# Kernel tuning notes

Hardware: AMD Instinct MI355X
Metric: run time of the kernel (lower is better)

The kernel has to match this reference:

```python
import jax, jax.numpy as jnp
import numpy as np

B, N, IN_F, H, DEG, L = 4096, 64, 32, 128, 8, 2
E = N * DEG
ALPHA = 0.2  # LeakyReLU slope
EPS = 1e-5   # LayerNorm eps


def setup_inputs() -> dict:
    key = jax.random.key(0)
    ks = jax.random.split(key, 16)
    # ring graph: node i -> (i+k) mod N for k=1..DEG (unique edges, every node has out-edges)
    src = jnp.repeat(jnp.arange(N, dtype=jnp.int32), DEG)
    dst = ((src + jnp.tile(jnp.arange(1, DEG + 1, dtype=jnp.int32), N)) % N).astype(jnp.int32)
    edge_index = jnp.stack([src, dst])  # (2, E)
    Hh = H // 2
    inp = {
        "x": jax.random.normal(ks[0], (B, IN_F), jnp.float32),
        "station_idx": jax.random.randint(ks[1], (B,), 0, N, jnp.int32),
        "edge_index": edge_index,
        "edge_weight": jax.random.uniform(ks[2], (E,), jnp.float32, 0.1, 1.0),
        "Wp": jax.random.normal(ks[3], (IN_F, H), jnp.float32) / np.sqrt(IN_F),
        "bp": jnp.zeros((H,), jnp.float32),
        "emb": jax.random.normal(ks[4], (N, Hh), jnp.float32) * 0.02,
        "gat_W": jax.random.normal(ks[5], (L, H, H), jnp.float32) / np.sqrt(H),
        "gat_a": jax.random.normal(ks[6], (L, 2 * H), jnp.float32) * 0.1,
        "W1": jax.random.normal(ks[7], (H + Hh, H), jnp.float32) / np.sqrt(H + Hh),
        "b1": jnp.zeros((H,), jnp.float32),
        "g1": jnp.ones((H,), jnp.float32),
        "be1": jnp.zeros((H,), jnp.float32),
        "W2": jax.random.normal(ks[8], (H, Hh), jnp.float32) / np.sqrt(H),
        "b2": jnp.zeros((Hh,), jnp.float32),
        "g2": jnp.ones((Hh,), jnp.float32),
        "be2": jnp.zeros((Hh,), jnp.float32),
        "Wo": jax.random.normal(ks[9], (Hh, 1), jnp.float32) / np.sqrt(Hh),
        "bo": jnp.zeros((1,), jnp.float32),
    }
    return inp


def _layernorm(v, g, b):
    m = v.mean(-1, keepdims=True)
    var = ((v - m) ** 2).mean(-1, keepdims=True)
    return (v - m) / jnp.sqrt(var + EPS) * g + b


def _gat(h, W, a, src, dst, edge_weight):
    # h: (B, N, H); W: (H, H); a: (2H,)
    Wh = jnp.einsum('bnf,fg->bng', h, W)
    s_src = Wh @ a[:H]   # (B, N)
    s_dst = Wh @ a[H:]   # (B, N)
    e = jax.nn.leaky_relu(s_src[:, src] + s_dst[:, dst], ALPHA)  # (B, E)
    e = e * edge_weight[None, :]
    att = jnp.zeros((h.shape[0], N, N), h.dtype).at[:, src, dst].set(e)
    mask = att == 0  # faithfully reproduces the torch zero-mask trick
    att = jnp.where(mask, -jnp.inf, att)
    att = jax.nn.softmax(att, axis=2)
    att = jnp.where(mask, 0.0, att)
    # dropout is identity at inference
    return jax.nn.elu(jnp.einsum('bnm,bmf->bnf', att, Wh))


def reference(x, station_idx, edge_index, edge_weight, Wp, bp, emb, gat_W, gat_a,
              W1, b1, g1, be1, W2, b2, g2, be2, Wo, bo):
    src, dst = edge_index[0], edge_index[1]
    h0 = x @ Wp + bp                               # (B, H)
    h = jnp.broadcast_to(h0[:, None, :], (x.shape[0], N, H))
    for i in range(L):
        h = h + _gat(h, gat_W[i], gat_a[i], src, dst, edge_weight)
    h_node = h[jnp.arange(x.shape[0]), station_idx]  # (B, H)
    s = emb[station_idx]                              # (B, H//2)
    z = jnp.concatenate([h_node, s], axis=-1)
    z = jax.nn.relu(_layernorm(z @ W1 + b1, g1, be1))
    z = jax.nn.relu(_layernorm(z @ W2 + b2, g2, be2))
    return (z @ Wo + bo).squeeze(-1)                  # (B,)
```

## Files before the change

### kernel.cpp

```cpp
#include <hip/hip_runtime.h>
#include <math.h>

namespace {

constexpr int INF = 32;
constexpr int H   = 128;
constexpr int HH  = 64;
constexpr int ZD  = 192;
constexpr int SPB = 4;
constexpr float LNEPS = 1e-5f;

__device__ __forceinline__ float elu1(float v) {
    return v > 0.f ? v : (__expf(v) - 1.f);
}

template<int DKq, int LDW, int NCOL>
__device__ __forceinline__ void gemm2(const float* __restrict__ W0,
                                      const float* __restrict__ act,
                                      float (&t)[SPB][NCOL])
{
    if constexpr (DKq == 8) {
        float w[8 * NCOL];
#pragma unroll
        for (int r = 0; r < 8; ++r)
#pragma unroll
            for (int c = 0; c < NCOL; ++c) w[r * NCOL + c] = W0[r * LDW + c * 64];
#pragma unroll
        for (int rr = 0; rr < 8; rr += 4) {
#pragma unroll
            for (int s = 0; s < SPB; ++s) {
                const float4 hv = *reinterpret_cast<const float4*>(act + s * ZD + rr);
#pragma unroll
                for (int c = 0; c < NCOL; ++c) {
                    t[s][c] += hv.x * w[(rr + 0) * NCOL + c] + hv.y * w[(rr + 1) * NCOL + c]
                             + hv.z * w[(rr + 2) * NCOL + c] + hv.w * w[(rr + 3) * NCOL + c];
                }
            }
        }
    } else {
        constexpr int NCH = DKq / 8;
        static_assert((NCH & 1) == 0, "even chunk count");
        float wa[8 * NCOL], wb[8 * NCOL];
#pragma unroll
        for (int r = 0; r < 8; ++r)
#pragma unroll
            for (int c = 0; c < NCOL; ++c) wa[r * NCOL + c] = W0[r * LDW + c * 64];
#pragma unroll
        for (int ch = 0; ch < NCH; ch += 2) {
#pragma unroll
            for (int r = 0; r < 8; ++r)
#pragma unroll
                for (int c = 0; c < NCOL; ++c)
                    wb[r * NCOL + c] = W0[((ch + 1) * 8 + r) * LDW + c * 64];
#pragma unroll
            for (int rr = 0; rr < 8; rr += 4) {
#pragma unroll
                for (int s = 0; s < SPB; ++s) {
                    const float4 hv = *reinterpret_cast<const float4*>(act + s * ZD + ch * 8 + rr);
#pragma unroll
                    for (int c = 0; c < NCOL; ++c) {
                        t[s][c] += hv.x * wa[(rr + 0) * NCOL + c] + hv.y * wa[(rr + 1) * NCOL + c]
                                 + hv.z * wa[(rr + 2) * NCOL + c] + hv.w * wa[(rr + 3) * NCOL + c];
                    }
                }
            }
            if (ch + 2 < NCH) {
#pragma unroll
                for (int r = 0; r < 8; ++r)
#pragma unroll
                    for (int c = 0; c < NCOL; ++c)
                        wa[r * NCOL + c] = W0[((ch + 2) * 8 + r) * LDW + c * 64];
            }
#pragma unroll
            for (int rr = 0; rr < 8; rr += 4) {
#pragma unroll
                for (int s = 0; s < SPB; ++s) {
                    const float4 hv = *reinterpret_cast<const float4*>(act + s * ZD + (ch + 1) * 8 + rr);
#pragma unroll
                    for (int c = 0; c < NCOL; ++c) {
                        t[s][c] += hv.x * wb[(rr + 0) * NCOL + c] + hv.y * wb[(rr + 1) * NCOL + c]
                                 + hv.z * wb[(rr + 2) * NCOL + c] + hv.w * wb[(rr + 3) * NCOL + c];
                    }
                }
            }
        }
    }
}

__global__ __launch_bounds__(256, 4) void fused_sthgat(
    const float* __restrict__ x, const int* __restrict__ sid,
    const float* __restrict__ Wp, const float* __restrict__ bp,
    const float* __restrict__ emb, const float* __restrict__ gatW,
    const float* __restrict__ W1, const float* __restrict__ b1,
    const float* __restrict__ g1, const float* __restrict__ be1,
    const float* __restrict__ W2, const float* __restrict__ b2,
    const float* __restrict__ g2, const float* __restrict__ be2,
    const float* __restrict__ Wo, const float* __restrict__ bo,
    float* __restrict__ out)
{
    __shared__ __align__(16) float P2[4 * SPB * H];
    __shared__ __align__(16) float buf0[SPB * ZD];
    __shared__ __align__(16) float buf1[SPB * ZD];

    const int tid  = threadIdx.x;
    const int lane = tid & 63;
    const int kq   = tid >> 6;
    const int c    = tid & 63;
    const int sw   = tid >> 6;
    const int sbase = blockIdx.x * SPB;

    if (tid < SPB * INF) {
        buf0[(tid >> 5) * ZD + (tid & 31)] = x[(size_t)sbase * INF + tid];
    }
    __syncthreads();

    {
        float t[SPB][2] = {};
        gemm2<8, H, 2>(Wp + (kq * 8) * H + c, buf0 + kq * 8, t);
#pragma unroll
        for (int s = 0; s < SPB; ++s) {
            P2[kq * (SPB * H) + s * H + c]      = t[s][0];
            P2[kq * (SPB * H) + s * H + c + 64] = t[s][1];
        }
        __syncthreads();
        float v0 = bp[c], v1 = bp[c + 64];
#pragma unroll
        for (int k = 0; k < 4; ++k) {
            v0 += P2[k * (SPB * H) + sw * H + c];
            v1 += P2[k * (SPB * H) + sw * H + c + 64];
        }
        buf1[sw * ZD + c]      = v0;
        buf1[sw * ZD + c + 64] = v1;
        __syncthreads();
    }

    {
        float t[SPB][2] = {};
        gemm2<32, H, 2>(gatW + (kq * 32) * H + c, buf1 + kq * 32, t);
#pragma unroll
        for (int s = 0; s < SPB; ++s) {
            P2[kq * (SPB * H) + s * H + c]      = t[s][0];
            P2[kq * (SPB * H) + s * H + c + 64] = t[s][1];
        }
        __syncthreads();
        float v0 = 0.f, v1 = 0.f;
#pragma unroll
        for (int k = 0; k < 4; ++k) {
            v0 += P2[k * (SPB * H) + sw * H + c];
            v1 += P2[k * (SPB * H) + sw * H + c + 64];
        }
        buf0[sw * ZD + c]      = buf1[sw * ZD + c]      + elu1(v0);
        buf0[sw * ZD + c + 64] = buf1[sw * ZD + c + 64] + elu1(v1);
        __syncthreads();
    }

    {
        float t[SPB][2] = {};
        gemm2<32, H, 2>(gatW + H * H + (kq * 32) * H + c, buf0 + kq * 32, t);
#pragma unroll
        for (int s = 0; s < SPB; ++s) {
            P2[kq * (SPB * H) + s * H + c]      = t[s][0];
            P2[kq * (SPB * H) + s * H + c + 64] = t[s][1];
        }
        __syncthreads();
        float v0 = 0.f, v1 = 0.f;
#pragma unroll
        for (int k = 0; k < 4; ++k) {
            v0 += P2[k * (SPB * H) + sw * H + c];
            v1 += P2[k * (SPB * H) + sw * H + c + 64];
        }
        buf1[sw * ZD + c]      = buf0[sw * ZD + c]      + elu1(v0);
        buf1[sw * ZD + c + 64] = buf0[sw * ZD + c + 64] + elu1(v1);
        {
            const int st = sid[sbase + sw];
            buf1[sw * ZD + H + c] = emb[st * HH + c];
        }
        __syncthreads();
    }

    {
        float t[SPB][2] = {};
        gemm2<48, H, 2>(W1 + (kq * 48) * H + c, buf1 + kq * 48, t);
#pragma unroll
        for (int s = 0; s < SPB; ++s) {
            P2[kq * (SPB * H) + s * H + c]      = t[s][0];
            P2[kq * (SPB * H) + s * H + c + 64] = t[s][1];
        }
        __syncthreads();
        float u0 = b1[c], u1 = b1[c + 64];
#pragma unroll
        for (int k = 0; k < 4; ++k) {
            u0 += P2[k * (SPB * H) + sw * H + c];
            u1 += P2[k * (SPB * H) + sw * H + c + 64];
        }
        float su = u0 + u1;
        float sq = u0 * u0 + u1 * u1;
#pragma unroll
        for (int off = 32; off >= 1; off >>= 1) {
            su += __shfl_xor(su, off, 64);
            sq += __shfl_xor(sq, off, 64);
        }
        const float m   = su * (1.f / H);
        const float var = sq * (1.f / H) - m * m;
        const float rs  = rsqrtf(var + LNEPS);
        buf0[sw * ZD + c]      = fmaxf((u0 - m) * rs * g1[c]      + be1[c],      0.f);
        buf0[sw * ZD + c + 64] = fmaxf((u1 - m) * rs * g1[c + 64] + be1[c + 64], 0.f);
        __syncthreads();
    }

    {
        float t[SPB][1] = {};
        gemm2<32, HH, 1>(W2 + (kq * 32) * HH + c, buf0 + kq * 32, t);
#pragma unroll
        for (int s = 0; s < SPB; ++s) {
            P2[kq * (SPB * HH) + s * HH + c] = t[s][0];
        }
        __syncthreads();
        float v = b2[c];
#pragma unroll
        for (int k = 0; k < 4; ++k) v += P2[k * (SPB * HH) + sw * HH + c];
        float su = v, sq = v * v;
#pragma unroll
        for (int off = 32; off >= 1; off >>= 1) {
            su += __shfl_xor(su, off, 64);
            sq += __shfl_xor(sq, off, 64);
        }
        const float m   = su * (1.f / HH);
        const float var = sq * (1.f / HH) - m * m;
        const float rs  = rsqrtf(var + LNEPS);
        const float z2  = fmaxf((v - m) * rs * g2[c] + be2[c], 0.f);
        float po = z2 * Wo[c];
#pragma unroll
        for (int off = 32; off >= 1; off >>= 1) po += __shfl_xor(po, off, 64);
        if (lane == 0) out[sbase + sw] = po + bo[0];
    }
}

}

extern "C" void kernel_launch(void* const* d_in, const int* in_sizes, int n_in,
                              void* d_out, int out_size, void* d_ws, size_t ws_size,
                              hipStream_t stream)
{
    const float* x    = (const float*)d_in[0];
    const int*   sid  = (const int*)d_in[1];
    const float* Wp   = (const float*)d_in[4];
    const float* bp   = (const float*)d_in[5];
    const float* emb  = (const float*)d_in[6];
    const float* gatW = (const float*)d_in[7];
    const float* W1   = (const float*)d_in[9];
    const float* b1   = (const float*)d_in[10];
    const float* g1   = (const float*)d_in[11];
    const float* be1  = (const float*)d_in[12];
    const float* W2   = (const float*)d_in[13];
    const float* b2   = (const float*)d_in[14];
    const float* g2   = (const float*)d_in[15];
    const float* be2  = (const float*)d_in[16];
    const float* Wo   = (const float*)d_in[17];
    const float* bo   = (const float*)d_in[18];
    float* out = (float*)d_out;

    dim3 grid(4096 / SPB);
    dim3 block(256);
    hipLaunchKernelGGL(fused_sthgat, grid, block, 0, stream,
                       x, sid, Wp, bp, emb, gatW, W1, b1, g1, be1,
                       W2, b2, g2, be2, Wo, bo, out);
}
```

Before: 104.8 us.

## Vectorize weight loads as float2 and triple-buffer weight prefetch in fused GEMMs

Result: slower. 108.4 us (+3.4%).

```diff
diff --git a/kernel.cpp b/kernel.cpp
--- a/kernel.cpp
+++ b/kernel.cpp
@@ -10,81 +10,114 @@
 constexpr int SPB = 4;
 constexpr float LNEPS = 1e-5f;
 
+template<int V> struct ic { static constexpr int value = V; };
+
+template<int N, int I = 0, class F>
+__device__ __forceinline__ void sfor(F&& f) {
+    if constexpr (I < N) { f(ic<I>{}); sfor<N, I + 1>(f); }
+}
+
 __device__ __forceinline__ float elu1(float v) {
     return v > 0.f ? v : (__expf(v) - 1.f);
 }
 
-template<int DKq, int LDW, int NCOL>
-__device__ __forceinline__ void gemm2(const float* __restrict__ W0,
-                                      const float* __restrict__ act,
-                                      float (&t)[SPB][NCOL])
+template<int DKq, int LDW>
+__device__ __forceinline__ void gemm_f2(const float* __restrict__ W0,
+                                        const float* __restrict__ actb,
+                                        float2 (&t)[SPB])
 {
-    if constexpr (DKq == 8) {
-        float w[8 * NCOL];
-#pragma unroll
-        for (int r = 0; r < 8; ++r)
-#pragma unroll
-            for (int c = 0; c < NCOL; ++c) w[r * NCOL + c] = W0[r * LDW + c * 64];
-#pragma unroll
-        for (int rr = 0; rr < 8; rr += 4) {
-#pragma unroll
-            for (int s = 0; s < SPB; ++s) {
-                const float4 hv = *reinterpret_cast<const float4*>(act + s * ZD + rr);
-#pragma unroll
-                for (int c = 0; c < NCOL; ++c) {
-                    t[s][c] += hv.x * w[(rr + 0) * NCOL + c] + hv.y * w[(rr + 1) * NCOL + c]
-                             + hv.z * w[(rr + 2) * NCOL + c] + hv.w * w[(rr + 3) * NCOL + c];
-                }
-            }
-        }
-    } else {
-        constexpr int NCH = DKq / 8;
-        static_assert((NCH & 1) == 0, "even chunk count");
-        float wa[8 * NCOL], wb[8 * NCOL];
-#pragma unroll
-        for (int r = 0; r < 8; ++r)
-#pragma unroll
-            for (int c = 0; c < NCOL; ++c) wa[r * NCOL + c] = W0[r * LDW + c * 64];
-#pragma unroll
-        for (int ch = 0; ch < NCH; ch += 2) {
-#pragma unroll
-            for (int r = 0; r < 8; ++r)
-#pragma unroll
-                for (int c = 0; c < NCOL; ++c)
-                    wb[r * NCOL + c] = W0[((ch + 1) * 8 + r) * LDW + c * 64];
-#pragma unroll
-            for (int rr = 0; rr < 8; rr += 4) {
-#pragma unroll
-                for (int s = 0; s < SPB; ++s) {
-                    const float4 hv = *reinterpret_cast<const float4*>(act + s * ZD + ch * 8 + rr);
-#pragma unroll
-                    for (int c = 0; c < NCOL; ++c) {
-                        t[s][c] += hv.x * wa[(rr + 0) * NCOL + c] + hv.y * wa[(rr + 1) * NCOL + c]
-                                 + hv.z * wa[(rr + 2) * NCOL + c] + hv.w * wa[(rr + 3) * NCOL + c];
-                    }
-                }
-            }
-            if (ch + 2 < NCH) {
-#pragma unroll
-                for (int r = 0; r < 8; ++r)
-#pragma unroll
-                    for (int c = 0; c < NCOL; ++c)
-                        wa[r * NCOL + c] = W0[((ch + 2) * 8 + r) * LDW + c * 64];
-            }
-#pragma unroll
-            for (int rr = 0; rr < 8; rr += 4) {
-#pragma unroll
-                for (int s = 0; s < SPB; ++s) {
-                    const float4 hv = *reinterpret_cast<const float4*>(act + s * ZD + (ch + 1) * 8 + rr);
-#pragma unroll
-                    for (int c = 0; c < NCOL; ++c) {
-                        t[s][c] += hv.x * wb[(rr + 0) * NCOL + c] + hv.y * wb[(rr + 1) * NCOL + c]
-                                 + hv.z * wb[(rr + 2) * NCOL + c] + hv.w * wb[(rr + 3) * NCOL + c];
-                    }
-                }
-            }
-        }
-    }
+    constexpr int NCH = DKq / 8;
+    float2 wA[8], wB[8], wC[8];
+
+    auto ld = [&](auto CH, float2 (&buf)[8]) {
+        constexpr int ch = decltype(CH)::value;
+        sfor<8>([&](auto R) {
+            buf[R.value] = *reinterpret_cast<const float2*>(
+                W0 + (size_t)(ch * 8 + R.value) * LDW);
+        });
+    };
+    auto comp = [&](auto CH, float2 (&buf)[8]) {
+        constexpr int ch = decltype(CH)::value;
+        sfor<2>([&](auto G) {
+            constexpr int g4 = decltype(G)::value;
+            constexpr int r0 = ch * 8 + g4 * 4;
+            float4 a[SPB];
+            sfor<SPB>([&](auto S) {
+                a[S.value] = *reinterpret_cast<const float4*>(
+                    actb + S.value * ZD + r0);
+            });
+            sfor<SPB>([&](auto S) {
+                constexpr int s = decltype(S)::value;
+                constexpr int rb = g4 * 4;
+                t[s].x += a[s].x * buf[rb + 0].x + a[s].y * buf[rb + 1].x
+                        + a[s].z * buf[rb + 2].x + a[s].w * buf[rb + 3].x;
+                t[s].y += a[s].x * buf[rb + 0].y + a[s].y * buf[rb + 1].y
+                        + a[s].z * buf[rb + 2].y + a[s].w * buf[rb + 3].y;
+            });
+        });
+    };
+
+    ld(ic<0>{}, wA);
+    if constexpr (NCH > 1) ld(ic<1>{}, wB);
+    sfor<NCH>([&](auto CH) {
+        constexpr int ch = decltype(CH)::value;
+        if constexpr (ch + 2 < NCH) {
+            if constexpr ((ch + 2) % 3 == 0)      ld(ic<ch + 2>{}, wA);
+            else if constexpr ((ch + 2) % 3 == 1) ld(ic<ch + 2>{}, wB);
+            else                                  ld(ic<ch + 2>{}, wC);
+        }
+        if constexpr (ch % 3 == 0)      comp(CH, wA);
+        else if constexpr (ch % 3 == 1) comp(CH, wB);
+        else                            comp(CH, wC);
+    });
+}
+
+template<int DKq, int LDW>
+__device__ __forceinline__ void gemm_s(const float* __restrict__ W0,
+                                       const float* __restrict__ actb,
+                                       float (&t)[SPB])
+{
+    constexpr int NCH = DKq / 8;
+    float wA[8], wB[8], wC[8];
+
+    auto ld = [&](auto CH, float (&buf)[8]) {
+        constexpr int ch = decltype(CH)::value;
+        sfor<8>([&](auto R) {
+            buf[R.value] = W0[(size_t)(ch * 8 + R.value) * LDW];
+        });
+    };
+    auto comp = [&](auto CH, float (&buf)[8]) {
+        constexpr int ch = decltype(CH)::value;
+        sfor<2>([&](auto G) {
+            constexpr int g4 = decltype(G)::value;
+            constexpr int r0 = ch * 8 + g4 * 4;
+            float4 a[SPB];
+            sfor<SPB>([&](auto S) {
+                a[S.value] = *reinterpret_cast<const float4*>(
+                    actb + S.value * ZD + r0);
+            });
+            sfor<SPB>([&](auto S) {
+                constexpr int s = decltype(S)::value;
+                constexpr int rb = g4 * 4;
+                t[s] += a[s].x * buf[rb + 0] + a[s].y * buf[rb + 1]
+                      + a[s].z * buf[rb + 2] + a[s].w * buf[rb + 3];
+            });
+        });
+    };
+
+    ld(ic<0>{}, wA);
+    if constexpr (NCH > 1) ld(ic<1>{}, wB);
+    sfor<NCH>([&](auto CH) {
+        constexpr int ch = decltype(CH)::value;
+        if constexpr (ch + 2 < NCH) {
+            if constexpr ((ch + 2) % 3 == 0)      ld(ic<ch + 2>{}, wA);
+            else if constexpr ((ch + 2) % 3 == 1) ld(ic<ch + 2>{}, wB);
+            else                                  ld(ic<ch + 2>{}, wC);
+        }
+        if constexpr (ch % 3 == 0)      comp(CH, wA);
+        else if constexpr (ch % 3 == 1) comp(CH, wB);
+        else                            comp(CH, wC);
+    });
 }
 
 __global__ __launch_bounds__(256, 4) void fused_sthgat(
@@ -109,90 +142,114 @@
     const int sw   = tid >> 6;
     const int sbase = blockIdx.x * SPB;
 
+    float2 wp[8];
+    sfor<8>([&](auto R) {
+        wp[R.value] = *reinterpret_cast<const float2*>(
+            Wp + (size_t)(kq * 8 + R.value) * H + 2 * c);
+    });
+    const float2 bpv = *reinterpret_cast<const float2*>(bp + 2 * c);
+
     if (tid < SPB * INF) {
         buf0[(tid >> 5) * ZD + (tid & 31)] = x[(size_t)sbase * INF + tid];
     }
     __syncthreads();
 
     {
-        float t[SPB][2] = {};
-        gemm2<8, H, 2>(Wp + (kq * 8) * H + c, buf0 + kq * 8, t);
-#pragma unroll
-        for (int s = 0; s < SPB; ++s) {
-            P2[kq * (SPB * H) + s * H + c]      = t[s][0];
-            P2[kq * (SPB * H) + s * H + c + 64] = t[s][1];
-        }
-        __syncthreads();
-        float v0 = bp[c], v1 = bp[c + 64];
-#pragma unroll
-        for (int k = 0; k < 4; ++k) {
-            v0 += P2[k * (SPB * H) + sw * H + c];
-            v1 += P2[k * (SPB * H) + sw * H + c + 64];
-        }
-        buf1[sw * ZD + c]      = v0;
-        buf1[sw * ZD + c + 64] = v1;
-        __syncthreads();
-    }
-
-    {
-        float t[SPB][2] = {};
-        gemm2<32, H, 2>(gatW + (kq * 32) * H + c, buf1 + kq * 32, t);
-#pragma unroll
-        for (int s = 0; s < SPB; ++s) {
-            P2[kq * (SPB * H) + s * H + c]      = t[s][0];
-            P2[kq * (SPB * H) + s * H + c + 64] = t[s][1];
-        }
-        __syncthreads();
-        float v0 = 0.f, v1 = 0.f;
-#pragma unroll
-        for (int k = 0; k < 4; ++k) {
-            v0 += P2[k * (SPB * H) + sw * H + c];
-            v1 += P2[k * (SPB * H) + sw * H + c + 64];
-        }
-        buf0[sw * ZD + c]      = buf1[sw * ZD + c]      + elu1(v0);
-        buf0[sw * ZD + c + 64] = buf1[sw * ZD + c + 64] + elu1(v1);
-        __syncthreads();
-    }
-
-    {
-        float t[SPB][2] = {};
-        gemm2<32, H, 2>(gatW + H * H + (kq * 32) * H + c, buf0 + kq * 32, t);
-#pragma unroll
-        for (int s = 0; s < SPB; ++s) {
-            P2[kq * (SPB * H) + s * H + c]      = t[s][0];
-            P2[kq * (SPB * H) + s * H + c + 64] = t[s][1];
-        }
-        __syncthreads();
-        float v0 = 0.f, v1 = 0.f;
-#pragma unroll
-        for (int k = 0; k < 4; ++k) {
-            v0 += P2[k * (SPB * H) + sw * H + c];
-            v1 += P2[k * (SPB * H) + sw * H + c + 64];
-        }
-        buf1[sw * ZD + c]      = buf0[sw * ZD + c]      + elu1(v0);
-        buf1[sw * ZD + c + 64] = buf0[sw * ZD + c + 64] + elu1(v1);
+        float2 t[SPB] = {};
+        const float* actb = buf0 + kq * 8;
+        sfor<2>([&](auto G) {
+            constexpr int g4 = decltype(G)::value;
+            float4 a[SPB];
+            sfor<SPB>([&](auto S) {
+                a[S.value] = *reinterpret_cast<const float4*>(
+                    actb + S.value * ZD + g4 * 4);
+            });
+            sfor<SPB>([&](auto S) {
+                constexpr int s = decltype(S)::value;
+                constexpr int rb = g4 * 4;
+                t[s].x += a[s].x * wp[rb + 0].x + a[s].y * wp[rb + 1].x
+                        + a[s].z * wp[rb + 2].x + a[s].w * wp[rb + 3].x;
+                t[s].y += a[s].x * wp[rb + 0].y + a[s].y * wp[rb + 1].y
+                        + a[s].z * wp[rb + 2].y + a[s].w * wp[rb + 3].y;
+            });
+        });
+        sfor<SPB>([&](auto S) {
+            *reinterpret_cast<float2*>(
+                P2 + kq * (SPB * H) + S.value * H + 2 * c) = t[S.value];
+        });
+        __syncthreads();
+        float2 v = bpv;
+        sfor<4>([&](auto K) {
+            const float2 p = *reinterpret_cast<const float2*>(
+                P2 + decltype(K)::value * (SPB * H) + sw * H + 2 * c);
+            v.x += p.x; v.y += p.y;
+        });
+        *reinterpret_cast<float2*>(buf1 + sw * ZD + 2 * c) = v;
+        __syncthreads();
+    }
+
+    {
+        float2 t[SPB] = {};
+        gemm_f2<32, H>(gatW + (size_t)(kq * 32) * H + 2 * c, buf1 + kq * 32, t);
+        sfor<SPB>([&](auto S) {
+            *reinterpret_cast<float2*>(
+                P2 + kq * (SPB * H) + S.value * H + 2 * c) = t[S.value];
+        });
+        __syncthreads();
+        float2 v = {0.f, 0.f};
+        sfor<4>([&](auto K) {
+            const float2 p = *reinterpret_cast<const float2*>(
+                P2 + decltype(K)::value * (SPB * H) + sw * H + 2 * c);
+            v.x += p.x; v.y += p.y;
+        });
+        const float2 hp = *reinterpret_cast<const float2*>(buf1 + sw * ZD + 2 * c);
+        float2 o; o.x = hp.x + elu1(v.x); o.y = hp.y + elu1(v.y);
+        *reinterpret_cast<float2*>(buf0 + sw * ZD + 2 * c) = o;
+        __syncthreads();
+    }
+
+    {
+        float2 t[SPB] = {};
+        gemm_f2<32, H>(gatW + (size_t)H * H + (size_t)(kq * 32) * H + 2 * c,
+                       buf0 + kq * 32, t);
+        sfor<SPB>([&](auto S) {
+            *reinterpret_cast<float2*>(
+                P2 + kq * (SPB * H) + S.value * H + 2 * c) = t[S.value];
+        });
+        __syncthreads();
+        float2 v = {0.f, 0.f};
+        sfor<4>([&](auto K) {
+            const float2 p = *reinterpret_cast<const float2*>(
+                P2 + decltype(K)::value * (SPB * H) + sw * H + 2 * c);
+            v.x += p.x; v.y += p.y;
+        });
+        const float2 hp = *reinterpret_cast<const float2*>(buf0 + sw * ZD + 2 * c);
+        float2 o; o.x = hp.x + elu1(v.x); o.y = hp.y + elu1(v.y);
+        *reinterpret_cast<float2*>(buf1 + sw * ZD + 2 * c) = o;
         {
             const int st = sid[sbase + sw];
-            buf1[sw * ZD + H + c] = emb[st * HH + c];
-        }
-        __syncthreads();
-    }
-
-    {
-        float t[SPB][2] = {};
-        gemm2<48, H, 2>(W1 + (kq * 48) * H + c, buf1 + kq * 48, t);
-#pragma unroll
-        for (int s = 0; s < SPB; ++s) {
-            P2[kq * (SPB * H) + s * H + c]      = t[s][0];
-            P2[kq * (SPB * H) + s * H + c + 64] = t[s][1];
-        }
-        __syncthreads();
-        float u0 = b1[c], u1 = b1[c + 64];
-#pragma unroll
-        for (int k = 0; k < 4; ++k) {
-            u0 += P2[k * (SPB * H) + sw * H + c];
-            u1 += P2[k * (SPB * H) + sw * H + c + 64];
-        }
+            buf1[sw * ZD + H + c] = emb[(size_t)st * HH + c];
+        }
+        __syncthreads();
+    }
+
+    {
+        const float2 b1v  = *reinterpret_cast<const float2*>(b1 + 2 * c);
+        const float2 g1v  = *reinterpret_cast<const float2*>(g1 + 2 * c);
+        const float2 be1v = *reinterpret_cast<const float2*>(be1 + 2 * c);
+        float2 t[SPB] = {};
+        gemm_f2<48, H>(W1 + (size_t)(kq * 48) * H + 2 * c, buf1 + kq * 48, t);
+        sfor<SPB>([&](auto S) {
+            *reinterpret_cast<float2*>(
+                P2 + kq * (SPB * H) + S.value * H + 2 * c) = t[S.value];
+        });
+        __syncthreads();
+        float u0 = b1v.x, u1 = b1v.y;
+        sfor<4>([&](auto K) {
+            const float2 p = *reinterpret_cast<const float2*>(
+                P2 + decltype(K)::value * (SPB * H) + sw * H + 2 * c);
+            u0 += p.x; u1 += p.y;
+        });
         float su = u0 + u1;
         float sq = u0 * u0 + u1 * u1;
 #pragma unroll
@@ -203,22 +260,29 @@
         const float m   = su * (1.f / H);
         const float var = sq * (1.f / H) - m * m;
         const float rs  = rsqrtf(var + LNEPS);
-        buf0[sw * ZD + c]      = fmaxf((u0 - m) * rs * g1[c]      + be1[c],      0.f);
-        buf0[sw * ZD + c + 64] = fmaxf((u1 - m) * rs * g1[c + 64] + be1[c + 64], 0.f);
-        __syncthreads();
-    }
-
-    {
-        float t[SPB][1] = {};
-        gemm2<32, HH, 1>(W2 + (kq * 32) * HH + c, buf0 + kq * 32, t);
-#pragma unroll
-        for (int s = 0; s < SPB; ++s) {
-            P2[kq * (SPB * HH) + s * HH + c] = t[s][0];
-        }
-        __syncthreads();
-        float v = b2[c];
-#pragma unroll
-        for (int k = 0; k < 4; ++k) v += P2[k * (SPB * HH) + sw * HH + c];
+        float2 z;
+        z.x = fmaxf((u0 - m) * rs * g1v.x + be1v.x, 0.f);
+        z.y = fmaxf((u1 - m) * rs * g1v.y + be1v.y, 0.f);
+        *reinterpret_cast<float2*>(buf0 + sw * ZD + 2 * c) = z;
+        __syncthreads();
+    }
+
+    {
+        const float b2v  = b2[c];
+        const float g2v  = g2[c];
+        const float be2v = be2[c];
+        const float wov  = Wo[c];
+        const float bov  = bo[0];
+        float t[SPB] = {};
+        gemm_s<32, HH>(W2 + (size_t)(kq * 32) * HH + c, buf0 + kq * 32, t);
+        sfor<SPB>([&](auto S) {
+            P2[kq * (SPB * HH) + S.value * HH + c] = t[S.value];
+        });
+        __syncthreads();
+        float v = b2v;
+        sfor<4>([&](auto K) {
+            v += P2[decltype(K)::value * (SPB * HH) + sw * HH + c];
+        });
         float su = v, sq = v * v;
 #pragma unroll
         for (int off = 32; off >= 1; off >>= 1) {
@@ -228,11 +292,11 @@
         const float m   = su * (1.f / HH);
         const float var = sq * (1.f / HH) - m * m;
         const float rs  = rsqrtf(var + LNEPS);
-        const float z2  = fmaxf((v - m) * rs * g2[c] + be2[c], 0.f);
-        float po = z2 * Wo[c];
+        const float z2  = fmaxf((v - m) * rs * g2v + be2v, 0.f);
+        float po = z2 * wov;
 #pragma unroll
         for (int off = 32; off >= 1; off >>= 1) po += __shfl_xor(po, off, 64);
-        if (lane == 0) out[sbase + sw] = po + bo[0];
+        if (lane == 0) out[sbase + sw] = po + bov;
     }
 }
 
```
